# Kernel tuning notes

Measured on AMD Instinct MI355X. Metric: run time of the kernel, lower is better.

## Reference

```python
import jax, jax.numpy as jnp
import numpy as np

N_RAYS = 65536   # 256x256 image
N_PTS = 128      # samples per ray
FEAT = 3         # RGB
FAR_DELTA = 1e10 # sentinel delta for last sample, as in the torch module


def setup_inputs() -> dict:
    key = jax.random.key(0)
    k1, k2, k3 = jax.random.split(key, 3)
    # depths along each ray must be increasing (deltas computed by diff)
    depth_values = jnp.sort(
        jax.random.uniform(k1, (N_RAYS, N_PTS), jnp.float32, 2.0, 6.0), axis=-1)
    density = jax.random.uniform(k2, (N_RAYS, N_PTS), jnp.float32)  # non-negative
    feature = jax.random.uniform(k3, (N_RAYS, N_PTS, FEAT), jnp.float32)
    return {"depth_values": depth_values, "density": density, "feature": feature}


def reference(depth_values, density, feature):
    n_rays, n_pts = depth_values.shape
    # deltas: consecutive depth differences, huge value appended for last bin
    deltas = jnp.concatenate(
        [depth_values[:, 1:] - depth_values[:, :-1],
         jnp.full((n_rays, 1), FAR_DELTA, depth_values.dtype)], axis=-1)
    tau = density * deltas                              # [n_rays, n_pts]
    # transmittance T_i = exp(-sum_{j<i} tau_j) (exclusive cumsum in log space)
    log_T = -jnp.concatenate(
        [jnp.zeros((n_rays, 1), tau.dtype), jnp.cumsum(tau[:, :-1], axis=-1)],
        axis=-1)
    weights = jnp.exp(log_T) * (1.0 - jnp.exp(-tau))    # [n_rays, n_pts]
    feat_out = jnp.einsum('np,npf->nf', weights, feature)         # [n_rays, F]
    depth_out = jnp.sum(weights * depth_values, axis=-1, keepdims=True)
    return jnp.concatenate([feat_out, depth_out], axis=-1)        # [n_rays, F+1]
```

## Files before the change

### kernel.cpp

```cpp
#include <hip/hip_runtime.h>

#define N_RAYS 65536
#define N_PTS 128
#define FEAT 3
#define FAR_DELTA 1e10f

__global__ __launch_bounds__(256) void volrend_kernel(
    const float* __restrict__ depth,
    const float* __restrict__ density,
    const float* __restrict__ feature,
    float* __restrict__ out)
{
    const int wave = threadIdx.x >> 6;
    const int lane = threadIdx.x & 63;
    const int ray  = (blockIdx.x << 2) + wave;

    const int base = ray * N_PTS;
    const float2 d   = *(const float2*)(depth   + base + 2 * lane);
    const float2 rho = *(const float2*)(density + base + 2 * lane);

    float next_dx = __shfl_down(d.x, 1);
    float delta_a = d.y - d.x;
    float delta_b = (lane == 63) ? FAR_DELTA : (next_dx - d.y);

    float tau_a = rho.x * delta_a;
    float tau_b = rho.y * delta_b;
    float pair  = tau_a + tau_b;

    float e = __shfl_up(pair, 1);
    if (lane == 0) e = 0.0f;
    #pragma unroll
    for (int off = 1; off < 64; off <<= 1) {
        float t = __shfl_up(e, off);
        if (lane >= off) e += t;
    }

    float Ta   = __expf(-e);
    float Tmid = __expf(-(e + tau_a));
    float Tend = __expf(-(e + tau_a + tau_b));
    float w_a = Ta - Tmid;
    float w_b = Tmid - Tend;

    const float2* f2 = (const float2*)(feature + (size_t)ray * (N_PTS * FEAT)
                                       + 6 * lane);
    float2 fa = f2[0];
    float2 fb = f2[1];
    float2 fc = f2[2];

    float acc0 = w_a * fa.x + w_b * fb.y;
    float acc1 = w_a * fa.y + w_b * fc.x;
    float acc2 = w_a * fb.x + w_b * fc.y;
    float acc3 = w_a * d.x  + w_b * d.y;

    #pragma unroll
    for (int off = 32; off > 0; off >>= 1) {
        acc0 += __shfl_down(acc0, off);
        acc1 += __shfl_down(acc1, off);
        acc2 += __shfl_down(acc2, off);
        acc3 += __shfl_down(acc3, off);
    }

    if (lane == 0) {
        *(float4*)(out + ray * 4) = make_float4(acc0, acc1, acc2, acc3);
    }
}

extern "C" void kernel_launch(void* const* d_in, const int* in_sizes, int n_in,
                              void* d_out, int out_size, void* d_ws, size_t ws_size,
                              hipStream_t stream) {
    const float* depth   = (const float*)d_in[0];
    const float* density = (const float*)d_in[1];
    const float* feature = (const float*)d_in[2];
    float* out = (float*)d_out;

    dim3 grid(N_RAYS / 4);
    dim3 block(256);
    volrend_kernel<<<grid, block, 0, stream>>>(depth, density, feature, out);
}
```

Before: 188.9 us.

## Stage feature loads through LDS with a persistent grid and four samples per lane

Each ray is now handled by 32 lanes with four samples per lane, using float4 loads for depth and density. The per-ray feature rows are loaded as fully coalesced float4 chunks into shared memory, then read back per lane. A fixed grid of 2048 blocks loops over ray groups, and the scan and reductions work on 32-lane halves of the wave. The aim is wider, coalesced global loads and less launch overhead, at the cost of extra LDS traffic and block-level barriers.

```diff
diff --git a/kernel.cpp b/kernel.cpp
--- a/kernel.cpp
+++ b/kernel.cpp
@@ -5,63 +5,81 @@
 #define FEAT 3
 #define FAR_DELTA 1e10f
 
-__global__ __launch_bounds__(256) void volrend_kernel(
+#define NBLOCKS 2048
+#define RAYS_PER_ITER 8
+#define NITERS (N_RAYS / (NBLOCKS * RAYS_PER_ITER))
+
+__global__ __launch_bounds__(256, 8) void volrend_kernel(
     const float* __restrict__ depth,
     const float* __restrict__ density,
     const float* __restrict__ feature,
     float* __restrict__ out)
 {
-    const int wave = threadIdx.x >> 6;
-    const int lane = threadIdx.x & 63;
-    const int ray  = (blockIdx.x << 2) + wave;
+    __shared__ float4 sfeat[RAYS_PER_ITER * (N_PTS * FEAT / 4)];
 
-    const int base = ray * N_PTS;
-    const float2 d   = *(const float2*)(depth   + base + 2 * lane);
-    const float2 rho = *(const float2*)(density + base + 2 * lane);
+    const int tid  = threadIdx.x;
+    const int sl   = tid & 31;
+    const int rloc = tid >> 5;
 
-    float next_dx = __shfl_down(d.x, 1);
-    float delta_a = d.y - d.x;
-    float delta_b = (lane == 63) ? FAR_DELTA : (next_dx - d.y);
+    for (int it = 0; it < NITERS; ++it) {
+        const int grp = (int)blockIdx.x + it * NBLOCKS;
+        const int ray = grp * RAYS_PER_ITER + rloc;
 
-    float tau_a = rho.x * delta_a;
-    float tau_b = rho.y * delta_b;
-    float pair  = tau_a + tau_b;
+        const float4 d   = *(const float4*)(depth   + ray * N_PTS + 4 * sl);
+        const float4 rho = *(const float4*)(density + ray * N_PTS + 4 * sl);
 
-    float e = __shfl_up(pair, 1);
-    if (lane == 0) e = 0.0f;
-    #pragma unroll
-    for (int off = 1; off < 64; off <<= 1) {
-        float t = __shfl_up(e, off);
-        if (lane >= off) e += t;
-    }
+        const float4* fsrc = (const float4*)feature
+                           + (size_t)grp * (RAYS_PER_ITER * 96) + tid;
+        float4 s0 = fsrc[0];
+        float4 s1 = fsrc[256];
+        float4 s2 = fsrc[512];
 
-    float Ta   = __expf(-e);
-    float Tmid = __expf(-(e + tau_a));
-    float Tend = __expf(-(e + tau_a + tau_b));
-    float w_a = Ta - Tmid;
-    float w_b = Tmid - Tend;
+        if (it) __syncthreads();
+        sfeat[tid]       = s0;
+        sfeat[tid + 256] = s1;
+        sfeat[tid + 512] = s2;
+        __syncthreads();
 
-    const float2* f2 = (const float2*)(feature + (size_t)ray * (N_PTS * FEAT)
-                                       + 6 * lane);
-    float2 fa = f2[0];
-    float2 fb = f2[1];
-    float2 fc = f2[2];
+        float nd = __shfl_down(d.x, 1);
+        float t0 = rho.x * (d.y - d.x);
+        float t1 = rho.y * (d.z - d.y);
+        float t2 = rho.z * (d.w - d.z);
+        float t3 = rho.w * ((sl == 31) ? FAR_DELTA : (nd - d.w));
+        float p1 = t0, p2 = p1 + t1, p3 = p2 + t2, tot = p3 + t3;
 
-    float acc0 = w_a * fa.x + w_b * fb.y;
-    float acc1 = w_a * fa.y + w_b * fc.x;
-    float acc2 = w_a * fb.x + w_b * fc.y;
-    float acc3 = w_a * d.x  + w_b * d.y;
+        float e = __shfl_up(tot, 1);
+        if (sl == 0) e = 0.0f;
+        #pragma unroll
+        for (int off = 1; off < 32; off <<= 1) {
+            float u = __shfl_up(e, off);
+            if (sl >= off) e += u;
+        }
 
-    #pragma unroll
-    for (int off = 32; off > 0; off >>= 1) {
-        acc0 += __shfl_down(acc0, off);
-        acc1 += __shfl_down(acc1, off);
-        acc2 += __shfl_down(acc2, off);
-        acc3 += __shfl_down(acc3, off);
-    }
+        float T0 = __expf(-e);
+        float T1 = __expf(-(e + p1));
+        float T2 = __expf(-(e + p2));
+        float T3 = __expf(-(e + p3));
+        float T4 = __expf(-(e + tot));
+        float w0 = T0 - T1, w1 = T1 - T2, w2 = T2 - T3, w3 = T3 - T4;
 
-    if (lane == 0) {
-        *(float4*)(out + ray * 4) = make_float4(acc0, acc1, acc2, acc3);
+        float acc3 = w0 * d.x + w1 * d.y + w2 * d.z + w3 * d.w;
+
+        const float4* frow = &sfeat[rloc * 96 + sl * 3];
+        float4 fa = frow[0], fb = frow[1], fc = frow[2];
+        float acc0 = w0 * fa.x + w1 * fa.w + w2 * fb.z + w3 * fc.y;
+        float acc1 = w0 * fa.y + w1 * fb.x + w2 * fb.w + w3 * fc.z;
+        float acc2 = w0 * fa.z + w1 * fb.y + w2 * fc.x + w3 * fc.w;
+
+        #pragma unroll
+        for (int off = 16; off > 0; off >>= 1) {
+            acc0 += __shfl_xor(acc0, off);
+            acc1 += __shfl_xor(acc1, off);
+            acc2 += __shfl_xor(acc2, off);
+            acc3 += __shfl_xor(acc3, off);
+        }
+        if (sl == 0) {
+            *(float4*)(out + ray * 4) = make_float4(acc0, acc1, acc2, acc3);
+        }
     }
 }
 
@@ -73,7 +91,7 @@
     const float* feature = (const float*)d_in[2];
     float* out = (float*)d_out;
 
-    dim3 grid(N_RAYS / 4);
+    dim3 grid(NBLOCKS);
     dim3 block(256);
     volrend_kernel<<<grid, block, 0, stream>>>(depth, density, feature, out);
 }
```

Result: slower. 193.9 us (+2.6%).

## Map one ray per thread with triple-buffered global-to-LDS prefetch pipeline

Applied to the files above, without the earlier changes.

Replaces the one-wave-per-ray shuffle scan and reduction with a sequential per-thread scan over each ray's samples. A three-slot global_load_lds pipeline streams depth, density and feature chunks of 16 bytes per lane directly into LDS, with explicit vmcnt waits to overlap loads with compute. This removes the cross-lane shuffle scan and reduction cost. In exchange, each load instruction hits 64 strided rays, so coalescing relies on cache reuse across chunks, and the grid shrinks to 256 blocks, which limits occupancy.

```diff
diff --git a/kernel.cpp b/kernel.cpp
--- a/kernel.cpp
+++ b/kernel.cpp
@@ -1,68 +1,97 @@
 #include <hip/hip_runtime.h>
 
 #define N_RAYS 65536
-#define N_PTS 128
-#define FEAT 3
+#define N_PTS  128
+#define FEAT   3
 #define FAR_DELTA 1e10f
 
-__global__ __launch_bounds__(256) void volrend_kernel(
+#define BLOCK  256
+#define NCHUNK 32
+#define SLOTS  5
+
+__global__ __launch_bounds__(BLOCK) void volrend_kernel(
     const float* __restrict__ depth,
     const float* __restrict__ density,
     const float* __restrict__ feature,
     float* __restrict__ out)
 {
-    const int wave = threadIdx.x >> 6;
-    const int lane = threadIdx.x & 63;
-    const int ray  = (blockIdx.x << 2) + wave;
+    __shared__ float4 sbuf[4][3][SLOTS][64];
 
-    const int base = ray * N_PTS;
-    const float2 d   = *(const float2*)(depth   + base + 2 * lane);
-    const float2 rho = *(const float2*)(density + base + 2 * lane);
+    const int tid = threadIdx.x;
+    const int w   = tid >> 6;
+    const int L   = tid & 63;
+    const int ray = (int)blockIdx.x * BLOCK + tid;
 
-    float next_dx = __shfl_down(d.x, 1);
-    float delta_a = d.y - d.x;
-    float delta_b = (lane == 63) ? FAR_DELTA : (next_dx - d.y);
+    const float* dp = depth   + (size_t)ray * N_PTS;
+    const float* rp = density + (size_t)ray * N_PTS;
+    const float* fp = feature + (size_t)ray * (N_PTS * FEAT);
 
-    float tau_a = rho.x * delta_a;
-    float tau_b = rho.y * delta_b;
-    float pair  = tau_a + tau_b;
+    float4 (*buf)[SLOTS][64] = sbuf[w];
 
-    float e = __shfl_up(pair, 1);
-    if (lane == 0) e = 0.0f;
-    #pragma unroll
-    for (int off = 1; off < 64; off <<= 1) {
-        float t = __shfl_up(e, off);
-        if (lane >= off) e += t;
+#define GLD(gp_, lp_)                                                         \
+    __builtin_amdgcn_global_load_lds(                                         \
+        (const __attribute__((address_space(1))) void*)(gp_),                 \
+        (__attribute__((address_space(3))) void*)(lp_), 16, 0, 0)
+
+#define ISSUE(c_, b_)                                                         \
+    do {                                                                      \
+        GLD(dp + (c_) * 4,      &buf[b_][0][0]);                              \
+        GLD(rp + (c_) * 4,      &buf[b_][1][0]);                              \
+        GLD(fp + (c_) * 12,     &buf[b_][2][0]);                              \
+        GLD(fp + (c_) * 12 + 4, &buf[b_][3][0]);                              \
+        GLD(fp + (c_) * 12 + 8, &buf[b_][4][0]);                              \
+    } while (0)
+
+    ISSUE(0, 0);
+    ISSUE(1, 1);
+
+    float cum = 0.0f, T = 1.0f;
+    float a0 = 0.f, a1 = 0.f, a2 = 0.f, a3 = 0.f;
+    float pd = 0.f, pr = 0.f, pf0 = 0.f, pf1 = 0.f, pf2 = 0.f;
+
+#define STEP(dv_, rv_, del_, fr_, fg_, fb_)                                   \
+    do {                                                                      \
+        float tau_ = (rv_) * (del_);                                          \
+        cum += tau_;                                                          \
+        float Tn_ = __expf(-cum);                                             \
+        float w_  = T - Tn_;                                                  \
+        a0 += w_ * (fr_); a1 += w_ * (fg_);                                   \
+        a2 += w_ * (fb_); a3 += w_ * (dv_);                                   \
+        T = Tn_;                                                              \
+    } while (0)
+
+#pragma unroll
+    for (int c = 0; c < NCHUNK; ++c) {
+        if (c + 2 < NCHUNK) ISSUE(c + 2, (c + 2) % 3);
+
+        if (c < NCHUNK - 2)       asm volatile("s_waitcnt vmcnt(10)" ::: "memory");
+        else if (c == NCHUNK - 2) asm volatile("s_waitcnt vmcnt(5)"  ::: "memory");
+        else                      asm volatile("s_waitcnt vmcnt(0)"  ::: "memory");
+
+        const int b = c % 3;
+        float4 dv = buf[b][0][L];
+        float4 rv = buf[b][1][L];
+        float4 f0 = buf[b][2][L];
+        float4 f1 = buf[b][3][L];
+        float4 f2 = buf[b][4][L];
+
+        if (c > 0) STEP(pd, pr, dv.x - pd, pf0, pf1, pf2);
+
+        STEP(dv.x, rv.x, dv.y - dv.x, f0.x, f0.y, f0.z);
+        STEP(dv.y, rv.y, dv.z - dv.y, f0.w, f1.x, f1.y);
+        STEP(dv.z, rv.z, dv.w - dv.z, f1.z, f1.w, f2.x);
+
+        pd  = dv.w;  pr  = rv.w;
+        pf0 = f2.y;  pf1 = f2.z;  pf2 = f2.w;
     }
 
-    float Ta   = __expf(-e);
-    float Tmid = __expf(-(e + tau_a));
-    float Tend = __expf(-(e + tau_a + tau_b));
-    float w_a = Ta - Tmid;
-    float w_b = Tmid - Tend;
+    STEP(pd, pr, FAR_DELTA, pf0, pf1, pf2);
 
-    const float2* f2 = (const float2*)(feature + (size_t)ray * (N_PTS * FEAT)
-                                       + 6 * lane);
-    float2 fa = f2[0];
-    float2 fb = f2[1];
-    float2 fc = f2[2];
+    *(float4*)(out + (size_t)ray * 4) = make_float4(a0, a1, a2, a3);
 
-    float acc0 = w_a * fa.x + w_b * fb.y;
-    float acc1 = w_a * fa.y + w_b * fc.x;
-    float acc2 = w_a * fb.x + w_b * fc.y;
-    float acc3 = w_a * d.x  + w_b * d.y;
-
-    #pragma unroll
-    for (int off = 32; off > 0; off >>= 1) {
-        acc0 += __shfl_down(acc0, off);
-        acc1 += __shfl_down(acc1, off);
-        acc2 += __shfl_down(acc2, off);
-        acc3 += __shfl_down(acc3, off);
-    }
-
-    if (lane == 0) {
-        *(float4*)(out + ray * 4) = make_float4(acc0, acc1, acc2, acc3);
-    }
+#undef STEP
+#undef ISSUE
+#undef GLD
 }
 
 extern "C" void kernel_launch(void* const* d_in, const int* in_sizes, int n_in,
@@ -73,7 +102,7 @@
     const float* feature = (const float*)d_in[2];
     float* out = (float*)d_out;
 
-    dim3 grid(N_RAYS / 4);
-    dim3 block(256);
+    dim3 grid(N_RAYS / BLOCK);
+    dim3 block(BLOCK);
     volrend_kernel<<<grid, block, 0, stream>>>(depth, density, feature, out);
 }
```

Result: slower. 229.8 us (+21.6%).
